# Optimization experiments

Hardware: AMD Instinct MI355X
Metric: run time of the kernel (lower is better)

## Reference

```python
import jax, jax.numpy as jnp
import numpy as np

N_NODES = 100000
N_EDGES = 6400000
IN_CH = 128
HID = 32


def setup_inputs() -> dict:
    key = jax.random.key(0)
    ks = jax.random.split(key, 12)
    x = jax.random.normal(ks[0], (N_NODES, IN_CH), dtype=jnp.float32)
    edge_index = jax.random.randint(ks[1], (2, N_EDGES), 0, N_NODES, dtype=jnp.int64)
    # Glorot-ish init for weights, zeros for biases (PyG / nn.Linear defaults vary,
    # values are random anyway for a correctness baseline)
    def w(k, fan_in, fan_out):
        s = 1.0 / np.sqrt(fan_in)
        return jax.random.uniform(k, (fan_in, fan_out), jnp.float32, -s, s)
    return {
        "x": x,
        "edge_index": edge_index,
        "W1": w(ks[2], IN_CH, HID), "b1": jnp.zeros((HID,), jnp.float32),
        "W2": w(ks[3], HID, HID),   "b2": jnp.zeros((HID,), jnp.float32),
        "Wl1": w(ks[4], HID, HID),  "bl1": jnp.zeros((HID,), jnp.float32),
        "Wl2": w(ks[5], HID, 1),    "bl2": jnp.zeros((1,), jnp.float32),
    }


def gcn_conv(x, W, b, src, dst, n_nodes):
    # GCNConv: h = x @ W; add self-loops; symmetric normalization D^-1/2 A_hat D^-1/2;
    # aggregate messages from src into dst; add bias.
    h = x @ W  # [N, out]
    loop = jnp.arange(n_nodes, dtype=src.dtype)
    src2 = jnp.concatenate([src, loop])
    dst2 = jnp.concatenate([dst, loop])
    ones = jnp.ones(src2.shape[0], dtype=h.dtype)
    deg = jax.ops.segment_sum(ones, dst2, num_segments=n_nodes)  # [N]
    dinv = jnp.where(deg > 0, jax.lax.rsqrt(deg), 0.0)
    norm = dinv[src2] * dinv[dst2]  # [E+N]
    msg = h[src2] * norm[:, None]   # [E+N, out]  (dominant memory traffic)
    out = jax.ops.segment_sum(msg, dst2, num_segments=n_nodes)
    return out + b


def reference(x, edge_index, W1, b1, W2, b2, Wl1, bl1, Wl2, bl2):
    src, dst = edge_index[0], edge_index[1]
    n = x.shape[0]
    h = jax.nn.relu(gcn_conv(x, W1, b1, src, dst, n))
    h = jax.nn.relu(gcn_conv(h, W2, b2, src, dst, n))
    h = jax.nn.relu(h @ Wl1 + bl1)
    return h @ Wl2 + bl2  # [N, 1]
```

## Files before the change

### kernel.cpp

```cpp
#include <hip/hip_runtime.h>

#define N_NODES 100000
#define N_EDGES 6400000
#define IN_CH   128
#define HID     32

#define BKT_SHIFT 9
#define BKT_MASK  511
#define BKT_SZ    512
#define NBKT      196
#define NBLK      1024
#define TILE      6250

#define O_EBUF 0u
#define O_HS   0u
#define O_HS2  12800000u
#define O_GH   25600000u
#define O_CUR  26402816u
#define O_CSR  25600000u
#define O_ROWS 51200000u
#define O_DINV 51700000u
#define O_BST  52200000u
#define O_BTOT 52300000u
#define O_FLAG 52400000u

__global__ void k_detect(const unsigned int* e, int* flag) {
    __shared__ int any;
    if (threadIdx.x == 0) any = 0;
    __syncthreads();
    int acc = 0;
    for (int i = threadIdx.x; i < 4096; i += 256)
        acc |= (e[2 * i + 1] != 0u);
    if (acc) atomicOr(&any, 1);
    __syncthreads();
    if (threadIdx.x == 0) *flag = any ? 0 : 1;
}

__device__ __forceinline__ int eload(const int* e, int is64, long long idx) {
    return is64 ? ((const int2*)e)[idx].x : e[(size_t)idx];
}

__global__ void k_hist(const int* e, const int* flag, int* ghist) {
    __shared__ int h[NBKT];
    for (int i = threadIdx.x; i < NBKT; i += 256) h[i] = 0;
    __syncthreads();
    int is64 = *flag;
    long long base = (long long)blockIdx.x * TILE;
    for (int k = threadIdx.x; k < TILE; k += 256) {
        int dst = eload(e, is64, (long long)N_EDGES + base + k);
        atomicAdd(&h[dst >> BKT_SHIFT], 1);
    }
    __syncthreads();
    int* g = ghist + blockIdx.x * NBKT;
    for (int i = threadIdx.x; i < NBKT; i += 256) g[i] = h[i];
}

__global__ void k_scan1(const int* __restrict__ ghist, int* __restrict__ btot) {
    int j = blockIdx.x * 256 + threadIdx.x;
    if (j >= NBKT) return;
    int t = 0;
    for (int blk = 0; blk < NBLK; ++blk) t += ghist[blk * NBKT + j];
    btot[j] = t;
}

__global__ void k_scan2(const int* __restrict__ btot, int* __restrict__ bstart) {
    __shared__ int s[1024];
    int t = threadIdx.x;
    int j0 = t * 2, j1 = t * 2 + 1;
    int a = (j0 < NBKT) ? btot[j0] : 0;
    int b = (j1 < NBKT) ? btot[j1] : 0;
    s[t] = a + b;
    __syncthreads();
    for (int off = 1; off < 1024; off <<= 1) {
        int v = (t >= off) ? s[t - off] : 0;
        __syncthreads();
        s[t] += v;
        __syncthreads();
    }
    int excl = s[t] - (a + b);
    if (j0 < NBKT) bstart[j0] = excl;
    if (j1 < NBKT) bstart[j1] = excl + a;
    if (t == 0) bstart[NBKT] = N_EDGES;
}

__global__ void k_scan3(const int* __restrict__ ghist, const int* __restrict__ bstart,
                        int* __restrict__ cursors) {
    int j = blockIdx.x * 256 + threadIdx.x;
    if (j >= NBKT) return;
    int run = bstart[j];
    for (int blk = 0; blk < NBLK; ++blk) {
        cursors[blk * NBKT + j] = run;
        run += ghist[blk * NBKT + j];
    }
}

__global__ void k_scatter(const int* e, const int* flag, const int* __restrict__ cursors,
                          unsigned int* __restrict__ ebuf) {
    __shared__ int cur[NBKT];
    const int* c = cursors + blockIdx.x * NBKT;
    for (int i = threadIdx.x; i < NBKT; i += 256) cur[i] = c[i];
    __syncthreads();
    int is64 = *flag;
    long long base = (long long)blockIdx.x * TILE;
    for (int k = threadIdx.x; k < TILE; k += 256) {
        int src = eload(e, is64, base + k);
        int dst = eload(e, is64, (long long)N_EDGES + base + k);
        int pos = atomicAdd(&cur[dst >> BKT_SHIFT], 1);
        ebuf[pos] = ((unsigned)src << BKT_SHIFT) | (unsigned)(dst & BKT_MASK);
    }
}

__launch_bounds__(512)
__global__ void k_sort2(const unsigned int* __restrict__ ebuf, const int* __restrict__ bstart,
                        int* __restrict__ csr, int* __restrict__ rows,
                        float* __restrict__ dinv) {
    __shared__ int hist[BKT_SZ];
    __shared__ int cur[BKT_SZ];
    __shared__ int wsum[8];
    int b = blockIdx.x;
    int s0 = bstart[b], e0 = bstart[b + 1];
    hist[threadIdx.x] = 0;
    __syncthreads();
    for (int i = s0 + threadIdx.x; i < e0; i += 512)
        atomicAdd(&hist[ebuf[i] & BKT_MASK], 1);
    __syncthreads();
    {
        int t = threadIdx.x;
        int lane = t & 63, w = t >> 6;
        int v = hist[t];
        int p = v;
#pragma unroll
        for (int off = 1; off < 64; off <<= 1) {
            int u = __shfl_up(p, off, 64);
            if (lane >= off) p += u;
        }
        if (lane == 63) wsum[w] = p;
        __syncthreads();
        int woff = 0;
        for (int k = 0; k < w; ++k) woff += wsum[k];
        int excl = s0 + woff + p - v;
        cur[t] = excl;
        int node = b * BKT_SZ + t;
        if (node <= N_NODES) rows[node] = excl;
        if (node < N_NODES)  dinv[node] = rsqrtf((float)(v + 1));
    }
    __syncthreads();
    for (int i = s0 + threadIdx.x; i < e0; i += 512) {
        unsigned v = ebuf[i];
        int pos = atomicAdd(&cur[v & BKT_MASK], 1);
        csr[pos] = (int)(v >> BKT_SHIFT);
    }
}

__launch_bounds__(256)
__global__ void k_gemm1(const float* __restrict__ x, const float* __restrict__ W1,
                        const float* __restrict__ dinv, float* __restrict__ hs) {
    __shared__ float w[IN_CH * HID];
    __shared__ float xs[8 * IN_CH];
    for (int i = threadIdx.x; i < IN_CH * HID; i += 256) w[i] = W1[i];
    const float4* xb = (const float4*)(x + (size_t)blockIdx.x * 8 * IN_CH);
    ((float4*)xs)[threadIdx.x] = xb[threadIdx.x];
    __syncthreads();
    int lane = threadIdx.x & 31, hw = threadIdx.x >> 5;
    int node = blockIdx.x * 8 + hw;
    const float* xr = xs + hw * IN_CH;
    float acc = 0.f;
#pragma unroll
    for (int k = 0; k < IN_CH; ++k) acc += xr[k] * w[k * HID + lane];
    hs[(size_t)node * HID + lane] = acc * dinv[node];
}

__launch_bounds__(256)
__global__ void k_agg1(const float* __restrict__ hs, const int* __restrict__ csr,
                       const int* __restrict__ rows, const float* __restrict__ dinv,
                       const float* __restrict__ b1, const float* __restrict__ W2,
                       float* __restrict__ hs2) {
    __shared__ float w2[HID * HID];
    __shared__ float h1s[8][HID];
    for (int i = threadIdx.x; i < HID * HID; i += 256) w2[i] = W2[i];
    int lane = threadIdx.x & 31, hw = threadIdx.x >> 5;
    int node = blockIdx.x * 8 + hw;
    int r0 = rows[node], r1 = rows[node + 1];
    float acc = hs[(size_t)node * HID + lane];
    int j = r0;
    for (; j + 8 <= r1; j += 8) {
        int t0 = csr[j + 0], t1 = csr[j + 1], t2 = csr[j + 2], t3 = csr[j + 3];
        int t4 = csr[j + 4], t5 = csr[j + 5], t6 = csr[j + 6], t7 = csr[j + 7];
        float f0 = hs[(size_t)t0 * HID + lane];
        float f1 = hs[(size_t)t1 * HID + lane];
        float f2 = hs[(size_t)t2 * HID + lane];
        float f3 = hs[(size_t)t3 * HID + lane];
        float f4 = hs[(size_t)t4 * HID + lane];
        float f5 = hs[(size_t)t5 * HID + lane];
        float f6 = hs[(size_t)t6 * HID + lane];
        float f7 = hs[(size_t)t7 * HID + lane];
        acc += ((f0 + f1) + (f2 + f3)) + ((f4 + f5) + (f6 + f7));
    }
    for (; j < r1; ++j) acc += hs[(size_t)csr[j] * HID + lane];
    float dv = dinv[node];
    h1s[hw][lane] = fmaxf(acc * dv + b1[lane], 0.f);
    __syncthreads();
    float a = 0.f;
#pragma unroll
    for (int k = 0; k < HID; ++k) a += h1s[hw][k] * w2[k * HID + lane];
    hs2[(size_t)node * HID + lane] = a * dv;
}

__launch_bounds__(256)
__global__ void k_agg2(const float* __restrict__ hs2, const int* __restrict__ csr,
                       const int* __restrict__ rows, const float* __restrict__ dinv,
                       const float* __restrict__ b2,
                       const float* __restrict__ Wl1, const float* __restrict__ bl1,
                       const float* __restrict__ Wl2, const float* __restrict__ bl2,
                       float* __restrict__ out) {
    __shared__ float wl1[HID * HID];
    __shared__ float h2s[8][HID];
    for (int i = threadIdx.x; i < HID * HID; i += 256) wl1[i] = Wl1[i];
    int lane = threadIdx.x & 31, hw = threadIdx.x >> 5;
    int node = blockIdx.x * 8 + hw;
    int r0 = rows[node], r1 = rows[node + 1];
    float acc = hs2[(size_t)node * HID + lane];
    int j = r0;
    for (; j + 8 <= r1; j += 8) {
        int t0 = csr[j + 0], t1 = csr[j + 1], t2 = csr[j + 2], t3 = csr[j + 3];
        int t4 = csr[j + 4], t5 = csr[j + 5], t6 = csr[j + 6], t7 = csr[j + 7];
        float f0 = hs2[(size_t)t0 * HID + lane];
        float f1 = hs2[(size_t)t1 * HID + lane];
        float f2 = hs2[(size_t)t2 * HID + lane];
        float f3 = hs2[(size_t)t3 * HID + lane];
        float f4 = hs2[(size_t)t4 * HID + lane];
        float f5 = hs2[(size_t)t5 * HID + lane];
        float f6 = hs2[(size_t)t6 * HID + lane];
        float f7 = hs2[(size_t)t7 * HID + lane];
        acc += ((f0 + f1) + (f2 + f3)) + ((f4 + f5) + (f6 + f7));
    }
    for (; j < r1; ++j) acc += hs2[(size_t)csr[j] * HID + lane];
    float h2 = fmaxf(acc * dinv[node] + b2[lane], 0.f);
    h2s[hw][lane] = h2;
    __syncthreads();
    float a = bl1[lane];
#pragma unroll
    for (int k = 0; k < HID; ++k) a += h2s[hw][k] * wl1[k * HID + lane];
    float o = fmaxf(a, 0.f) * Wl2[lane];
#pragma unroll
    for (int off = 16; off; off >>= 1) o += __shfl_down(o, off, 32);
    if (lane == 0) out[node] = o + *bl2;
}

extern "C" void kernel_launch(void* const* d_in, const int* in_sizes, int n_in,
                              void* d_out, int out_size, void* d_ws, size_t ws_size,
                              hipStream_t stream) {
    const float* x   = (const float*)d_in[0];
    const int*   e   = (const int*)d_in[1];
    const float* W1  = (const float*)d_in[2];
    const float* b1  = (const float*)d_in[3];
    const float* W2  = (const float*)d_in[4];
    const float* b2  = (const float*)d_in[5];
    const float* Wl1 = (const float*)d_in[6];
    const float* bl1 = (const float*)d_in[7];
    const float* Wl2 = (const float*)d_in[8];
    const float* bl2 = (const float*)d_in[9];
    float* out = (float*)d_out;

    char* w = (char*)d_ws;
    unsigned int* ebuf    = (unsigned int*)(w + O_EBUF);
    float*        hs      = (float*)(w + O_HS);
    float*        hs2     = (float*)(w + O_HS2);
    int*          ghist   = (int*)(w + O_GH);
    int*          cursors = (int*)(w + O_CUR);
    int*          csr     = (int*)(w + O_CSR);
    int*          rows    = (int*)(w + O_ROWS);
    float*        dinv    = (float*)(w + O_DINV);
    int*          bstart  = (int*)(w + O_BST);
    int*          btot    = (int*)(w + O_BTOT);
    int*          flag    = (int*)(w + O_FLAG);

    const int NB_BIN  = (NBKT + 255) / 256;
    const int NB_NODE = N_NODES / 8;

    k_detect<<<1, 256, 0, stream>>>((const unsigned int*)e, flag);
    k_hist<<<NBLK, 256, 0, stream>>>(e, flag, ghist);
    k_scan1<<<NB_BIN, 256, 0, stream>>>(ghist, btot);
    k_scan2<<<1, 1024, 0, stream>>>(btot, bstart);
    k_scan3<<<NB_BIN, 256, 0, stream>>>(ghist, bstart, cursors);
    k_scatter<<<NBLK, 256, 0, stream>>>(e, flag, cursors, ebuf);
    k_sort2<<<NBKT, 512, 0, stream>>>(ebuf, bstart, csr, rows, dinv);

    k_gemm1<<<NB_NODE, 256, 0, stream>>>(x, W1, dinv, hs);
    k_agg1<<<NB_NODE, 256, 0, stream>>>(hs, csr, rows, dinv, b1, W2, hs2);
    k_agg2<<<NB_NODE, 256, 0, stream>>>(hs2, csr, rows, dinv, b2,
                                        Wl1, bl1, Wl2, bl2, out);
}
```

Baseline: 454.8 us.

## Partition aggregation by source-node chunks with 16-bit CSR indices

The CSR is re-bucketed so each destination node's neighbours are grouped into four source-range chunks of 25000 nodes, and each chunk's sources are stored as 16-bit offsets. Aggregation then runs as four passes per layer, each gathering only from a 3.2 MB slice of the feature table, and keeps a running sum in a global accumulator buffer. The aim is to keep the random gather working set cache-resident and to halve index traffic. In exchange it adds extra kernel launches and extra read/write passes over the accumulator per layer.

```diff
diff --git a/kernel.cpp b/kernel.cpp
--- a/kernel.cpp
+++ b/kernel.cpp
@@ -11,6 +11,8 @@
 #define NBKT      196
 #define NBLK      1024
 #define TILE      6250
+#define NCHUNK    4
+#define CBASE     25000
 
 #define O_EBUF 0u
 #define O_HS   0u
@@ -18,11 +20,12 @@
 #define O_GH   25600000u
 #define O_CUR  26402816u
 #define O_CSR  25600000u
-#define O_ROWS 51200000u
-#define O_DINV 51700000u
-#define O_BST  52200000u
-#define O_BTOT 52300000u
-#define O_FLAG 52400000u
+#define O_ROWS4 38400000u
+#define O_CNT4  40000000u
+#define O_DINV  41600000u
+#define O_BST   42000000u
+#define O_BTOT  42002048u
+#define O_FLAG  42004096u
 
 __global__ void k_detect(const unsigned int* e, int* flag) {
     __shared__ int any;
@@ -66,20 +69,16 @@
 __global__ void k_scan2(const int* __restrict__ btot, int* __restrict__ bstart) {
     __shared__ int s[1024];
     int t = threadIdx.x;
-    int j0 = t * 2, j1 = t * 2 + 1;
-    int a = (j0 < NBKT) ? btot[j0] : 0;
-    int b = (j1 < NBKT) ? btot[j1] : 0;
-    s[t] = a + b;
+    int v = (t < NBKT) ? btot[t] : 0;
+    s[t] = v;
     __syncthreads();
     for (int off = 1; off < 1024; off <<= 1) {
-        int v = (t >= off) ? s[t - off] : 0;
+        int u = (t >= off) ? s[t - off] : 0;
         __syncthreads();
-        s[t] += v;
+        s[t] += u;
         __syncthreads();
     }
-    int excl = s[t] - (a + b);
-    if (j0 < NBKT) bstart[j0] = excl;
-    if (j1 < NBKT) bstart[j1] = excl + a;
+    if (t < NBKT) bstart[t] = s[t] - v;
     if (t == 0) bstart[NBKT] = N_EDGES;
 }
 
@@ -112,23 +111,29 @@
 
 __launch_bounds__(512)
 __global__ void k_sort2(const unsigned int* __restrict__ ebuf, const int* __restrict__ bstart,
-                        int* __restrict__ csr, int* __restrict__ rows,
-                        float* __restrict__ dinv) {
-    __shared__ int hist[BKT_SZ];
-    __shared__ int cur[BKT_SZ];
+                        unsigned short* __restrict__ csr16, int* __restrict__ rows4,
+                        int* __restrict__ cnt4, float* __restrict__ dinv) {
+    __shared__ int hist[NCHUNK * BKT_SZ];
+    __shared__ int cur[NCHUNK * BKT_SZ];
     __shared__ int wsum[8];
     int b = blockIdx.x;
     int s0 = bstart[b], e0 = bstart[b + 1];
-    hist[threadIdx.x] = 0;
-    __syncthreads();
-    for (int i = s0 + threadIdx.x; i < e0; i += 512)
-        atomicAdd(&hist[ebuf[i] & BKT_MASK], 1);
-    __syncthreads();
+    int t = threadIdx.x;
+#pragma unroll
+    for (int i = 0; i < NCHUNK; ++i) hist[i * 512 + t] = 0;
+    __syncthreads();
+    for (int i = s0 + t; i < e0; i += 512) {
+        unsigned v = ebuf[i];
+        int src = (int)(v >> BKT_SHIFT);
+        int c = src / CBASE;
+        atomicAdd(&hist[c * 512 + (v & BKT_MASK)], 1);
+    }
+    __syncthreads();
+    int c0 = hist[4 * t + 0], c1 = hist[4 * t + 1], c2 = hist[4 * t + 2], c3 = hist[4 * t + 3];
+    int ssum = c0 + c1 + c2 + c3;
     {
-        int t = threadIdx.x;
         int lane = t & 63, w = t >> 6;
-        int v = hist[t];
-        int p = v;
+        int p = ssum;
 #pragma unroll
         for (int off = 1; off < 64; off <<= 1) {
             int u = __shfl_up(p, off, 64);
@@ -138,17 +143,38 @@
         __syncthreads();
         int woff = 0;
         for (int k = 0; k < w; ++k) woff += wsum[k];
-        int excl = s0 + woff + p - v;
-        cur[t] = excl;
+        int excl = woff + p - ssum;
+        int e0b = s0 + excl;
+        int e1b = e0b + c0, e2b = e1b + c1, e3b = e2b + c2;
+        cur[4 * t + 0] = e0b; cur[4 * t + 1] = e1b;
+        cur[4 * t + 2] = e2b; cur[4 * t + 3] = e3b;
+        int starts[4] = {e0b, e1b, e2b, e3b};
+        int cnts[4]   = {c0, c1, c2, c3};
+#pragma unroll
+        for (int i = 0; i < 4; ++i) {
+            int bin = 4 * t + i;
+            int c = bin >> 9, dl = bin & BKT_MASK;
+            int node = b * BKT_SZ + dl;
+            if (node < N_NODES) {
+                rows4[c * N_NODES + node] = starts[i];
+                cnt4[c * N_NODES + node]  = cnts[i];
+            }
+        }
+    }
+    __syncthreads();
+    {
         int node = b * BKT_SZ + t;
-        if (node <= N_NODES) rows[node] = excl;
-        if (node < N_NODES)  dinv[node] = rsqrtf((float)(v + 1));
-    }
-    __syncthreads();
-    for (int i = s0 + threadIdx.x; i < e0; i += 512) {
+        if (node < N_NODES) {
+            int deg = hist[t] + hist[512 + t] + hist[1024 + t] + hist[1536 + t];
+            dinv[node] = rsqrtf((float)(deg + 1));
+        }
+    }
+    for (int i = s0 + t; i < e0; i += 512) {
         unsigned v = ebuf[i];
-        int pos = atomicAdd(&cur[v & BKT_MASK], 1);
-        csr[pos] = (int)(v >> BKT_SHIFT);
+        int src = (int)(v >> BKT_SHIFT);
+        int c = src / CBASE;
+        int pos = atomicAdd(&cur[c * 512 + (v & BKT_MASK)], 1);
+        csr16[pos] = (unsigned short)(src - c * CBASE);
     }
 }
 
@@ -171,21 +197,56 @@
 }
 
 __launch_bounds__(256)
-__global__ void k_agg1(const float* __restrict__ hs, const int* __restrict__ csr,
-                       const int* __restrict__ rows, const float* __restrict__ dinv,
-                       const float* __restrict__ b1, const float* __restrict__ W2,
-                       float* __restrict__ hs2) {
+__global__ void k_agg_pass(const float* __restrict__ feat, float* __restrict__ acc,
+                           const unsigned short* __restrict__ csr16,
+                           const int* __restrict__ rows4p, const int* __restrict__ cnt4p,
+                           int cbase, int first) {
+    int lane = threadIdx.x & 31, hw = threadIdx.x >> 5;
+    int node = blockIdx.x * 8 + hw;
+    float a = first ? feat[(size_t)node * HID + lane]
+                    : acc[(size_t)node * HID + lane];
+    int start = rows4p[node], len = cnt4p[node];
+    const unsigned short* cs = csr16 + start;
+    int j = 0;
+    for (; j + 8 <= len; j += 8) {
+        int t0 = cbase + cs[j + 0], t1 = cbase + cs[j + 1];
+        int t2 = cbase + cs[j + 2], t3 = cbase + cs[j + 3];
+        int t4 = cbase + cs[j + 4], t5 = cbase + cs[j + 5];
+        int t6 = cbase + cs[j + 6], t7 = cbase + cs[j + 7];
+        float f0 = feat[(size_t)t0 * HID + lane];
+        float f1 = feat[(size_t)t1 * HID + lane];
+        float f2 = feat[(size_t)t2 * HID + lane];
+        float f3 = feat[(size_t)t3 * HID + lane];
+        float f4 = feat[(size_t)t4 * HID + lane];
+        float f5 = feat[(size_t)t5 * HID + lane];
+        float f6 = feat[(size_t)t6 * HID + lane];
+        float f7 = feat[(size_t)t7 * HID + lane];
+        a += ((f0 + f1) + (f2 + f3)) + ((f4 + f5) + (f6 + f7));
+    }
+    for (; j < len; ++j) a += feat[(size_t)(cbase + cs[j]) * HID + lane];
+    acc[(size_t)node * HID + lane] = a;
+}
+
+__launch_bounds__(256)
+__global__ void k_agg1_final(const float* __restrict__ hs, float* __restrict__ acc,
+                             const unsigned short* __restrict__ csr16,
+                             const int* __restrict__ rows4p, const int* __restrict__ cnt4p,
+                             int cbase, const float* __restrict__ dinv,
+                             const float* __restrict__ b1, const float* __restrict__ W2) {
     __shared__ float w2[HID * HID];
     __shared__ float h1s[8][HID];
     for (int i = threadIdx.x; i < HID * HID; i += 256) w2[i] = W2[i];
     int lane = threadIdx.x & 31, hw = threadIdx.x >> 5;
     int node = blockIdx.x * 8 + hw;
-    int r0 = rows[node], r1 = rows[node + 1];
-    float acc = hs[(size_t)node * HID + lane];
-    int j = r0;
-    for (; j + 8 <= r1; j += 8) {
-        int t0 = csr[j + 0], t1 = csr[j + 1], t2 = csr[j + 2], t3 = csr[j + 3];
-        int t4 = csr[j + 4], t5 = csr[j + 5], t6 = csr[j + 6], t7 = csr[j + 7];
+    float a = acc[(size_t)node * HID + lane];
+    int start = rows4p[node], len = cnt4p[node];
+    const unsigned short* cs = csr16 + start;
+    int j = 0;
+    for (; j + 8 <= len; j += 8) {
+        int t0 = cbase + cs[j + 0], t1 = cbase + cs[j + 1];
+        int t2 = cbase + cs[j + 2], t3 = cbase + cs[j + 3];
+        int t4 = cbase + cs[j + 4], t5 = cbase + cs[j + 5];
+        int t6 = cbase + cs[j + 6], t7 = cbase + cs[j + 7];
         float f0 = hs[(size_t)t0 * HID + lane];
         float f1 = hs[(size_t)t1 * HID + lane];
         float f2 = hs[(size_t)t2 * HID + lane];
@@ -194,36 +255,41 @@
         float f5 = hs[(size_t)t5 * HID + lane];
         float f6 = hs[(size_t)t6 * HID + lane];
         float f7 = hs[(size_t)t7 * HID + lane];
-        acc += ((f0 + f1) + (f2 + f3)) + ((f4 + f5) + (f6 + f7));
-    }
-    for (; j < r1; ++j) acc += hs[(size_t)csr[j] * HID + lane];
+        a += ((f0 + f1) + (f2 + f3)) + ((f4 + f5) + (f6 + f7));
+    }
+    for (; j < len; ++j) a += hs[(size_t)(cbase + cs[j]) * HID + lane];
     float dv = dinv[node];
-    h1s[hw][lane] = fmaxf(acc * dv + b1[lane], 0.f);
-    __syncthreads();
-    float a = 0.f;
-#pragma unroll
-    for (int k = 0; k < HID; ++k) a += h1s[hw][k] * w2[k * HID + lane];
-    hs2[(size_t)node * HID + lane] = a * dv;
+    h1s[hw][lane] = fmaxf(a * dv + b1[lane], 0.f);
+    __syncthreads();
+    float g = 0.f;
+#pragma unroll
+    for (int k = 0; k < HID; ++k) g += h1s[hw][k] * w2[k * HID + lane];
+    acc[(size_t)node * HID + lane] = g * dv;
 }
 
 __launch_bounds__(256)
-__global__ void k_agg2(const float* __restrict__ hs2, const int* __restrict__ csr,
-                       const int* __restrict__ rows, const float* __restrict__ dinv,
-                       const float* __restrict__ b2,
-                       const float* __restrict__ Wl1, const float* __restrict__ bl1,
-                       const float* __restrict__ Wl2, const float* __restrict__ bl2,
-                       float* __restrict__ out) {
+__global__ void k_agg2_final(const float* __restrict__ hs2, const float* __restrict__ acc,
+                             const unsigned short* __restrict__ csr16,
+                             const int* __restrict__ rows4p, const int* __restrict__ cnt4p,
+                             int cbase, const float* __restrict__ dinv,
+                             const float* __restrict__ b2,
+                             const float* __restrict__ Wl1, const float* __restrict__ bl1,
+                             const float* __restrict__ Wl2, const float* __restrict__ bl2,
+                             float* __restrict__ out) {
     __shared__ float wl1[HID * HID];
     __shared__ float h2s[8][HID];
     for (int i = threadIdx.x; i < HID * HID; i += 256) wl1[i] = Wl1[i];
     int lane = threadIdx.x & 31, hw = threadIdx.x >> 5;
     int node = blockIdx.x * 8 + hw;
-    int r0 = rows[node], r1 = rows[node + 1];
-    float acc = hs2[(size_t)node * HID + lane];
-    int j = r0;
-    for (; j + 8 <= r1; j += 8) {
-        int t0 = csr[j + 0], t1 = csr[j + 1], t2 = csr[j + 2], t3 = csr[j + 3];
-        int t4 = csr[j + 4], t5 = csr[j + 5], t6 = csr[j + 6], t7 = csr[j + 7];
+    float a = acc[(size_t)node * HID + lane];
+    int start = rows4p[node], len = cnt4p[node];
+    const unsigned short* cs = csr16 + start;
+    int j = 0;
+    for (; j + 8 <= len; j += 8) {
+        int t0 = cbase + cs[j + 0], t1 = cbase + cs[j + 1];
+        int t2 = cbase + cs[j + 2], t3 = cbase + cs[j + 3];
+        int t4 = cbase + cs[j + 4], t5 = cbase + cs[j + 5];
+        int t6 = cbase + cs[j + 6], t7 = cbase + cs[j + 7];
         float f0 = hs2[(size_t)t0 * HID + lane];
         float f1 = hs2[(size_t)t1 * HID + lane];
         float f2 = hs2[(size_t)t2 * HID + lane];
@@ -232,16 +298,16 @@
         float f5 = hs2[(size_t)t5 * HID + lane];
         float f6 = hs2[(size_t)t6 * HID + lane];
         float f7 = hs2[(size_t)t7 * HID + lane];
-        acc += ((f0 + f1) + (f2 + f3)) + ((f4 + f5) + (f6 + f7));
-    }
-    for (; j < r1; ++j) acc += hs2[(size_t)csr[j] * HID + lane];
-    float h2 = fmaxf(acc * dinv[node] + b2[lane], 0.f);
+        a += ((f0 + f1) + (f2 + f3)) + ((f4 + f5) + (f6 + f7));
+    }
+    for (; j < len; ++j) a += hs2[(size_t)(cbase + cs[j]) * HID + lane];
+    float h2 = fmaxf(a * dinv[node] + b2[lane], 0.f);
     h2s[hw][lane] = h2;
     __syncthreads();
-    float a = bl1[lane];
-#pragma unroll
-    for (int k = 0; k < HID; ++k) a += h2s[hw][k] * wl1[k * HID + lane];
-    float o = fmaxf(a, 0.f) * Wl2[lane];
+    float g = bl1[lane];
+#pragma unroll
+    for (int k = 0; k < HID; ++k) g += h2s[hw][k] * wl1[k * HID + lane];
+    float o = fmaxf(g, 0.f) * Wl2[lane];
 #pragma unroll
     for (int off = 16; off; off >>= 1) o += __shfl_down(o, off, 32);
     if (lane == 0) out[node] = o + *bl2;
@@ -263,31 +329,42 @@
     float* out = (float*)d_out;
 
     char* w = (char*)d_ws;
-    unsigned int* ebuf    = (unsigned int*)(w + O_EBUF);
-    float*        hs      = (float*)(w + O_HS);
-    float*        hs2     = (float*)(w + O_HS2);
-    int*          ghist   = (int*)(w + O_GH);
-    int*          cursors = (int*)(w + O_CUR);
-    int*          csr     = (int*)(w + O_CSR);
-    int*          rows    = (int*)(w + O_ROWS);
-    float*        dinv    = (float*)(w + O_DINV);
-    int*          bstart  = (int*)(w + O_BST);
-    int*          btot    = (int*)(w + O_BTOT);
-    int*          flag    = (int*)(w + O_FLAG);
-
-    const int NB_BIN  = (NBKT + 255) / 256;
+    unsigned int*   ebuf    = (unsigned int*)(w + O_EBUF);
+    float*          hs      = (float*)(w + O_HS);
+    float*          hs2     = (float*)(w + O_HS2);
+    int*            ghist   = (int*)(w + O_GH);
+    int*            cursors = (int*)(w + O_CUR);
+    unsigned short* csr16   = (unsigned short*)(w + O_CSR);
+    int*            rows4   = (int*)(w + O_ROWS4);
+    int*            cnt4    = (int*)(w + O_CNT4);
+    float*          dinv    = (float*)(w + O_DINV);
+    int*            bstart  = (int*)(w + O_BST);
+    int*            btot    = (int*)(w + O_BTOT);
+    int*            flag    = (int*)(w + O_FLAG);
+
     const int NB_NODE = N_NODES / 8;
 
     k_detect<<<1, 256, 0, stream>>>((const unsigned int*)e, flag);
     k_hist<<<NBLK, 256, 0, stream>>>(e, flag, ghist);
-    k_scan1<<<NB_BIN, 256, 0, stream>>>(ghist, btot);
+    k_scan1<<<1, 256, 0, stream>>>(ghist, btot);
     k_scan2<<<1, 1024, 0, stream>>>(btot, bstart);
-    k_scan3<<<NB_BIN, 256, 0, stream>>>(ghist, bstart, cursors);
+    k_scan3<<<1, 256, 0, stream>>>(ghist, bstart, cursors);
     k_scatter<<<NBLK, 256, 0, stream>>>(e, flag, cursors, ebuf);
-    k_sort2<<<NBKT, 512, 0, stream>>>(ebuf, bstart, csr, rows, dinv);
+    k_sort2<<<NBKT, 512, 0, stream>>>(ebuf, bstart, csr16, rows4, cnt4, dinv);
 
     k_gemm1<<<NB_NODE, 256, 0, stream>>>(x, W1, dinv, hs);
-    k_agg1<<<NB_NODE, 256, 0, stream>>>(hs, csr, rows, dinv, b1, W2, hs2);
-    k_agg2<<<NB_NODE, 256, 0, stream>>>(hs2, csr, rows, dinv, b2,
-                                        Wl1, bl1, Wl2, bl2, out);
-}
+
+    for (int p = 0; p < NCHUNK - 1; ++p)
+        k_agg_pass<<<NB_NODE, 256, 0, stream>>>(hs, hs2, csr16,
+            rows4 + p * N_NODES, cnt4 + p * N_NODES, p * CBASE, p == 0);
+    k_agg1_final<<<NB_NODE, 256, 0, stream>>>(hs, hs2, csr16,
+        rows4 + (NCHUNK - 1) * N_NODES, cnt4 + (NCHUNK - 1) * N_NODES,
+        (NCHUNK - 1) * CBASE, dinv, b1, W2);
+
+    for (int p = 0; p < NCHUNK - 1; ++p)
+        k_agg_pass<<<NB_NODE, 256, 0, stream>>>(hs2, hs, csr16,
+            rows4 + p * N_NODES, cnt4 + p * N_NODES, p * CBASE, p == 0);
+    k_agg2_final<<<NB_NODE, 256, 0, stream>>>(hs2, hs, csr16,
+        rows4 + (NCHUNK - 1) * N_NODES, cnt4 + (NCHUNK - 1) * N_NODES,
+        (NCHUNK - 1) * CBASE, dinv, b2, Wl1, bl1, Wl2, bl2, out);
+}
```

After: 553.0 us. +21.6%, slower.
